# Optimization experiments

Hardware: AMD Instinct MI355X
Metric: run time of the kernel (lower is better)

Reference implementation:

```python
import jax, jax.numpy as jnp
import numpy as np

N_NODES = 10000
N_EDGES = 160000
MUL0 = 16   # multiplicity of 0e irreps
MUL1 = 8    # multiplicity of 1o irreps
H_EDGE = 64
W_NUMEL = MUL0*MUL0 + MUL0*MUL1 + MUL1*MUL1 + MUL1*MUL0  # 576
EPS = 1e-5


def setup_inputs() -> dict:
    key = jax.random.key(0)
    ks = jax.random.split(key, 10)
    atom_features = jax.random.normal(ks[0], (N_NODES, MUL0 + 3*MUL1), dtype=jnp.float32)
    edge_features = jax.random.normal(ks[1], (N_EDGES, H_EDGE), dtype=jnp.float32)
    edge_sh = jax.random.normal(ks[2], (N_EDGES, 4), dtype=jnp.float32)
    edge_index = jax.random.randint(ks[3], (2, N_EDGES), 0, N_NODES, dtype=jnp.int32)
    # fc: Linear(h_edge,h_edge) -> ReLU -> Linear(h_edge, weight_numel)
    fc_w1 = jax.random.normal(ks[4], (H_EDGE, H_EDGE), dtype=jnp.float32) / np.sqrt(H_EDGE).astype(np.float32)
    fc_b1 = jnp.zeros((H_EDGE,), jnp.float32)
    fc_w2 = jax.random.normal(ks[5], (H_EDGE, W_NUMEL), dtype=jnp.float32) / np.sqrt(H_EDGE).astype(np.float32)
    fc_b2 = jnp.zeros((W_NUMEL,), jnp.float32)
    # e3nn BatchNorm affine params: one weight per (mul,irrep) channel, bias only for scalars
    bn_weight = jnp.ones((MUL0 + MUL1,), jnp.float32)
    bn_bias = jnp.zeros((MUL0,), jnp.float32)
    return {"atom_features": atom_features, "edge_features": edge_features,
            "edge_sh": edge_sh, "edge_index": edge_index,
            "fc_w1": fc_w1, "fc_b1": fc_b1, "fc_w2": fc_w2, "fc_b2": fc_b2,
            "bn_weight": bn_weight, "bn_bias": bn_bias}


def _tensor_product(x, edge_sh, w):
    # x: [E, 40] gathered node features; edge_sh: [E, 4]; w: [E, 576] per-edge weights
    E = x.shape[0]
    x0 = x[:, :MUL0]                       # [E,16] scalars 0e
    x1 = x[:, MUL0:].reshape(E, MUL1, 3)   # [E,8,3] vectors 1o
    sh0 = edge_sh[:, 0]                    # [E]
    sh1 = edge_sh[:, 1:4]                  # [E,3]
    i0 = 0
    w11 = w[:, i0:i0+MUL0*MUL0].reshape(E, MUL0, MUL0); i0 += MUL0*MUL0  # 0e x 0e -> 0e
    w12 = w[:, i0:i0+MUL0*MUL1].reshape(E, MUL0, MUL1); i0 += MUL0*MUL1  # 0e x 1o -> 1o
    w13 = w[:, i0:i0+MUL1*MUL1].reshape(E, MUL1, MUL1); i0 += MUL1*MUL1  # 1o x 0e -> 1o
    w14 = w[:, i0:i0+MUL1*MUL0].reshape(E, MUL1, MUL0)                   # 1o x 1o -> 0e (dot)
    inv = lambda f: np.float32(1.0/np.sqrt(f))
    out0 = (jnp.einsum('ei,eij->ej', x0 * sh0[:, None], w11) * inv(MUL0)
            + jnp.einsum('eim,em,eij->ej', x1, sh1, w14) * inv(3*MUL1))
    out1 = (jnp.einsum('ei,em,eij->ejm', x0, sh1, w12) * inv(MUL0)
            + jnp.einsum('eim,eij->ejm', x1 * sh0[:, None, None], w13) * inv(MUL1))
    return jnp.concatenate([out0, out1.reshape(E, MUL1*3)], axis=-1)  # [E,40]


def _batch_norm_irreps(x, bn_weight, bn_bias):
    # e3nn BatchNorm (training mode, batch stats): center+normalize scalars, norm-normalize vectors
    n = x.shape[0]
    s = x[:, :MUL0]                          # [N,16]
    v = x[:, MUL0:].reshape(n, MUL1, 3)      # [N,8,3]
    s = s - s.mean(axis=0)
    s_norm = (s * s).mean(axis=0)            # per scalar channel
    s = s * (jax.lax.rsqrt(s_norm + EPS) * bn_weight[:MUL0]) + bn_bias
    v_norm = (v * v).mean(axis=-1).mean(axis=0)   # per vector channel
    v = v * (jax.lax.rsqrt(v_norm + EPS) * bn_weight[MUL0:])[None, :, None]
    return jnp.concatenate([s, v.reshape(n, MUL1*3)], axis=-1)


def reference(atom_features, edge_features, edge_sh, edge_index,
              fc_w1, fc_b1, fc_w2, fc_b2, bn_weight, bn_bias):
    edge_dst = edge_index[0]
    edge_src = edge_index[1]
    # per-edge TP weights from edge features
    h = jax.nn.relu(edge_features @ fc_w1 + fc_b1)
    w = h @ fc_w2 + fc_b2                              # [E, 576]
    # gather -> tensor product
    tp = _tensor_product(atom_features[edge_dst], edge_sh, w)  # [E,40]
    # scatter_mean over source nodes with dim_size = n_nodes
    sums = jax.ops.segment_sum(tp, edge_src, num_segments=N_NODES)
    cnts = jax.ops.segment_sum(jnp.ones((tp.shape[0],), tp.dtype), edge_src, num_segments=N_NODES)
    out = sums / jnp.maximum(cnts, 1.0)[:, None]
    # residual (in/out irreps have the same dim -> zero padding)
    out = out + atom_features
    out = _batch_norm_irreps(out, bn_weight, bn_bias)
    return out
```

## Files before the change

### kernel.cpp

```cpp
#include <hip/hip_runtime.h>
#include <hip/hip_bf16.h>

#define N_NODES 10000
#define N_EDGES 160000
#define MUL0 16
#define MUL1 8
#define H_EDGE 64
#define W_NUMEL 576
#define EPS 1e-5f

#define BM 32
#define THREADS 256
#define WP 592
#define XS 52
#define CAP 32

#define INV16 0.25f
#define INV24 0.20412414523193154f
#define INV8  0.3535533905932738f

typedef __attribute__((ext_vector_type(8))) short bf16x8;
typedef __attribute__((ext_vector_type(4))) short bf16x4;
typedef __attribute__((ext_vector_type(4))) float f32x4;

__device__ __forceinline__ unsigned short f2bf(float x) {
    __hip_bfloat16 h = __float2bfloat16(x);
    return __builtin_bit_cast(unsigned short, h);
}
__device__ __forceinline__ float bf2f(unsigned short u) {
    union { unsigned int i; float f; } c; c.i = ((unsigned int)u) << 16; return c.f;
}
__device__ __forceinline__ float dot8(bf16x8 w, f32x4 a, f32x4 b) {
    float s = bf2f((unsigned short)w[0]) * a[0];
    s = fmaf(bf2f((unsigned short)w[1]), a[1], s);
    s = fmaf(bf2f((unsigned short)w[2]), a[2], s);
    s = fmaf(bf2f((unsigned short)w[3]), a[3], s);
    s = fmaf(bf2f((unsigned short)w[4]), b[0], s);
    s = fmaf(bf2f((unsigned short)w[5]), b[1], s);
    s = fmaf(bf2f((unsigned short)w[6]), b[2], s);
    s = fmaf(bf2f((unsigned short)w[7]), b[3], s);
    return s;
}

__device__ __forceinline__ int perm_n(int colp) {
    if (colp < 256)      { int jj = colp >> 4,        ii = colp & 15;        return 16 * ii + jj; }
    else if (colp < 384) { int t = colp - 256; int jj = t >> 4, ii = t & 15; return 256 + 8 * ii + jj; }
    else if (colp < 448) { int t = colp - 384; int jj = t >> 3, ii = t & 7;  return 384 + 8 * ii + jj; }
    else                 { int t = colp - 448; int jj = t >> 3, ii = t & 7;  return 448 + 16 * ii + jj; }
}

__global__ __launch_bounds__(256)
void prep_frags(const float* __restrict__ W1, const float* __restrict__ W2,
                const float* __restrict__ b2, const int* __restrict__ e_src,
                unsigned short* __restrict__ W1F, unsigned short* __restrict__ W2F,
                float* __restrict__ b2p, int* __restrict__ cnt_i,
                int* __restrict__ slots)
{
    const int idx = blockIdx.x * 256 + threadIdx.x;
    if (idx < 4096) {
        const int j = idx & 7, l = (idx >> 3) & 63, ks = (idx >> 9) & 1, mt = idx >> 10;
        const int k = 32 * ks + 16 * (j >> 2) + 4 * (l >> 4) + (j & 3);
        const int col = 16 * mt + (l & 15);
        W1F[idx] = f2bf(W1[k * 64 + col]);
    } else if (idx < 4096 + 36864) {
        const int i2 = idx - 4096;
        const int j = i2 & 7, l = (i2 >> 3) & 63, ks = (i2 >> 9) & 1, nt = i2 >> 10;
        const int k = 32 * ks + 16 * (j >> 2) + 4 * (l >> 4) + (j & 3);
        const int colp = 16 * nt + (l & 15);
        W2F[i2] = f2bf(W2[k * 576 + perm_n(colp)]);
    } else if (idx < 4096 + 36864 + 576) {
        const int np = idx - 40960;
        b2p[np] = b2[perm_n(np)];
    }
    if (idx < N_EDGES) {
        const int src = e_src[idx];
        const int pos = atomicAdd(&cnt_i[src], 1);
        if (pos < CAP) slots[src * CAP + pos] = idx;
    }
}

__global__ __launch_bounds__(THREADS)
void fused_edge_kernel(const float* __restrict__ atom,
                       const float* __restrict__ ef,
                       const float* __restrict__ esh,
                       const int*   __restrict__ e_dst,
                       const unsigned short* __restrict__ W1F,
                       const float* __restrict__ b1,
                       const unsigned short* __restrict__ W2F,
                       const float* __restrict__ b2p,
                       unsigned short* __restrict__ tp)
{
    __shared__ __align__(16) unsigned short W_lds[16 * WP];
    __shared__ __align__(16) float xstage[32 * XS];
    __shared__ __align__(16) unsigned short pack_lds[16 * 40];
    unsigned short* ef_lds = W_lds;

    const int tid = threadIdx.x;
    const int l   = tid & 63;
    const int wv  = tid >> 6;
    const int e0  = blockIdx.x * BM;
    const int h4  = l >> 4;
    const int e16 = l & 15;
    const int el  = tid >> 4;
    const int j   = tid & 15;
    const int j8  = j & 7;

    float4 efv[2];
    #pragma unroll
    for (int rr = 0; rr < 2; ++rr) {
        const int i = tid + rr * 256;
        efv[rr] = *(const float4*)(ef + (size_t)(e0 + (i >> 4)) * 64 + (i & 15) * 4);
    }

    int dstP[2]; float4 shvP[2];
    #pragma unroll
    for (int mt = 0; mt < 2; ++mt) {
        const int e = e0 + 16 * mt + el;
        dstP[mt] = e_dst[e];
        shvP[mt] = *(const float4*)(esh + (size_t)e * 4);
    }

    float xjP[2], v0P[2], v1P[2], v2P[2];
    #pragma unroll
    for (int mt = 0; mt < 2; ++mt) {
        const float* x = atom + (size_t)dstP[mt] * 40;
        xjP[mt] = x[j];
        v0P[mt] = x[16 + 3 * j8];
        v1P[mt] = x[17 + 3 * j8];
        v2P[mt] = x[18 + 3 * j8];
    }

    #pragma unroll
    for (int rr = 0; rr < 2; ++rr) {
        const int i    = tid + rr * 256;
        const int edge = i >> 4;
        const int f    = (i & 15) * 4;
        bf16x4 p;
        p[0] = (short)f2bf(efv[rr].x); p[1] = (short)f2bf(efv[rr].y);
        p[2] = (short)f2bf(efv[rr].z); p[3] = (short)f2bf(efv[rr].w);
        const int addr = ((edge << 7) + (f << 1)) ^ ((edge & 7) << 4);
        *(bf16x4*)((char*)ef_lds + addr) = p;
    }
    __syncthreads();

    bf16x8 bH[2][2];
    #pragma unroll
    for (int et = 0; et < 2; ++et) {
        const int edge = 16 * et + e16;
        bf16x8 bE[2];
        #pragma unroll
        for (int ks = 0; ks < 2; ++ks) {
            const int f0 = 32 * ks + 4 * h4;
            const int a0 = ((edge << 7) + (f0 << 1)) ^ ((edge & 7) << 4);
            const int a1 = ((edge << 7) + ((f0 + 16) << 1)) ^ ((edge & 7) << 4);
            bf16x4 lo = *(const bf16x4*)((const char*)ef_lds + a0);
            bf16x4 hi = *(const bf16x4*)((const char*)ef_lds + a1);
            bf16x8 b;
            b[0]=lo[0]; b[1]=lo[1]; b[2]=lo[2]; b[3]=lo[3];
            b[4]=hi[0]; b[5]=hi[1]; b[6]=hi[2]; b[7]=hi[3];
            bE[ks] = b;
        }
        f32x4 accG[4];
        #pragma unroll
        for (int mti = 0; mti < 4; ++mti) {
            accG[mti] = *(const f32x4*)(b1 + 16 * mti + 4 * h4);
            #pragma unroll
            for (int ks = 0; ks < 2; ++ks) {
                const bf16x8 aW = *(const bf16x8*)(W1F + ((size_t)(mti * 2 + ks) * 64 + l) * 8);
                accG[mti] = __builtin_amdgcn_mfma_f32_16x16x32_bf16(aW, bE[ks], accG[mti], 0, 0, 0);
            }
        }
        #pragma unroll
        for (int ks = 0; ks < 2; ++ks) {
            bf16x8 b;
            #pragma unroll
            for (int jj = 0; jj < 4; ++jj) {
                b[jj]     = (short)f2bf(fmaxf(accG[2 * ks    ][jj], 0.0f));
                b[jj + 4] = (short)f2bf(fmaxf(accG[2 * ks + 1][jj], 0.0f));
            }
            bH[et][ks] = b;
        }
    }

    float sh0P[2], s1xP[2], s1yP[2], s1zP[2];
    #pragma unroll
    for (int mt = 0; mt < 2; ++mt) {
        sh0P[mt] = shvP[mt].x; s1xP[mt] = shvP[mt].y;
        s1yP[mt] = shvP[mt].z; s1zP[mt] = shvP[mt].w;
        float* xrow = xstage + (16 * mt + el) * XS;
        xrow[j] = xjP[mt];
        if (j < 8) {
            xrow[16 + j] = v0P[mt] * shvP[mt].y + v1P[mt] * shvP[mt].z + v2P[mt] * shvP[mt].w;
            xrow[24 + j] = v0P[mt];
            xrow[32 + j] = v1P[mt];
            xrow[40 + j] = v2P[mt];
        }
    }
    __syncthreads();

    bf16x4 accb[9][2];
    #pragma unroll
    for (int t = 0; t < 9; ++t) {
        const int nt = 9 * wv + t;
        const f32x4 bias = *(const f32x4*)(b2p + 16 * nt + 4 * h4);
        f32x4 a0 = bias, a1 = bias;
        #pragma unroll
        for (int ks = 0; ks < 2; ++ks) {
            const bf16x8 aW = *(const bf16x8*)(W2F + ((size_t)(nt * 2 + ks) * 64 + l) * 8);
            a0 = __builtin_amdgcn_mfma_f32_16x16x32_bf16(aW, bH[0][ks], a0, 0, 0, 0);
            a1 = __builtin_amdgcn_mfma_f32_16x16x32_bf16(aW, bH[1][ks], a1, 0, 0, 0);
        }
        #pragma unroll
        for (int r = 0; r < 4; ++r) {
            accb[t][0][r] = (short)f2bf(a0[r]);
            accb[t][1][r] = (short)f2bf(a1[r]);
        }
    }

    #pragma unroll
    for (int mt = 0; mt < 2; ++mt) {
        #pragma unroll
        for (int t = 0; t < 9; ++t) {
            const int nt = 9 * wv + t;
            *(bf16x4*)&W_lds[e16 * WP + 16 * nt + 4 * h4] = accb[t][mt];
        }
        __syncthreads();

        const unsigned short* Wt = W_lds + el * WP;
        const float* xv = xstage + (16 * mt + el) * XS;
        const float sh0 = sh0P[mt], s1x = s1xP[mt], s1y = s1yP[mt], s1z = s1zP[mt];

        const bf16x8 t0a = *(const bf16x8*)(Wt + 16 * j);
        const bf16x8 t0b = *(const bf16x8*)(Wt + 16 * j + 8);
        const bf16x8 t3  = *(const bf16x8*)(Wt + 448 + 8 * j);
        const f32x4 xa = *(const f32x4*)(xv);
        const f32x4 xb = *(const f32x4*)(xv + 4);
        const f32x4 xc = *(const f32x4*)(xv + 8);
        const f32x4 xd = *(const f32x4*)(xv + 12);
        const f32x4 d0 = *(const f32x4*)(xv + 16);
        const f32x4 d1 = *(const f32x4*)(xv + 20);
        const float s1 = dot8(t0a, xa, xb) + dot8(t0b, xc, xd);
        const float s2 = dot8(t3, d0, d1);
        pack_lds[el * 40 + j] = f2bf(INV16 * sh0 * s1 + INV24 * s2);
        if (j < 8) {
            const bf16x8 t1a = *(const bf16x8*)(Wt + 256 + 16 * j);
            const bf16x8 t1b = *(const bf16x8*)(Wt + 256 + 16 * j + 8);
            const bf16x8 t2  = *(const bf16x8*)(Wt + 384 + 8 * j);
            const f32x4 v0a = *(const f32x4*)(xv + 24), v0b = *(const f32x4*)(xv + 28);
            const f32x4 v1a = *(const f32x4*)(xv + 32), v1b = *(const f32x4*)(xv + 36);
            const f32x4 v2a = *(const f32x4*)(xv + 40), v2b = *(const f32x4*)(xv + 44);
            const float p  = dot8(t1a, xa, xb) + dot8(t1b, xc, xd);
            const float q0 = dot8(t2, v0a, v0b);
            const float q1 = dot8(t2, v1a, v1b);
            const float q2 = dot8(t2, v2a, v2b);
            const float ps = INV16 * p, qs = INV8 * sh0;
            pack_lds[el * 40 + 16 + 3 * j + 0] = f2bf(s1x * ps + qs * q0);
            pack_lds[el * 40 + 16 + 3 * j + 1] = f2bf(s1y * ps + qs * q1);
            pack_lds[el * 40 + 16 + 3 * j + 2] = f2bf(s1z * ps + qs * q2);
        }
        __syncthreads();

        if (tid < 80) {
            const bf16x8 c = *(const bf16x8*)(pack_lds + 8 * tid);
            *(bf16x8*)(tp + (size_t)(e0 + 16 * mt) * 40 + 8 * tid) = c;
        }
    }
}

__global__ __launch_bounds__(256)
void gather_stats_kernel(const int* __restrict__ cnt_i, const int* __restrict__ slots,
                         const unsigned short* __restrict__ tp, const float* __restrict__ atom,
                         float* __restrict__ y, float* __restrict__ stats)
{
    __shared__ float sred[40];
    const int t0 = blockIdx.x * 256 + threadIdx.x;
    if (threadIdx.x < 40) sred[threadIdx.x] = 0.0f;
    __syncthreads();

    if (t0 < N_NODES * 10) {
        const int n = t0 / 10, g = t0 % 10;
        const int cnt = cnt_i[n];
        const int m = min(cnt, CAP);
        float a0 = 0.f, a1 = 0.f, a2 = 0.f, a3 = 0.f;
        int i = 0;
        for (; i + 4 <= m; i += 4) {
            const int4 e4 = *(const int4*)(slots + n * CAP + i);
            const ushort4 va = *(const ushort4*)(tp + (size_t)e4.x * 40 + 4 * g);
            const ushort4 vb = *(const ushort4*)(tp + (size_t)e4.y * 40 + 4 * g);
            const ushort4 vc = *(const ushort4*)(tp + (size_t)e4.z * 40 + 4 * g);
            const ushort4 vd = *(const ushort4*)(tp + (size_t)e4.w * 40 + 4 * g);
            a0 += bf2f(va.x) + bf2f(vb.x) + bf2f(vc.x) + bf2f(vd.x);
            a1 += bf2f(va.y) + bf2f(vb.y) + bf2f(vc.y) + bf2f(vd.y);
            a2 += bf2f(va.z) + bf2f(vb.z) + bf2f(vc.z) + bf2f(vd.z);
            a3 += bf2f(va.w) + bf2f(vb.w) + bf2f(vc.w) + bf2f(vd.w);
        }
        for (; i < m; ++i) {
            const int eid = slots[n * CAP + i];
            const ushort4 v = *(const ushort4*)(tp + (size_t)eid * 40 + 4 * g);
            a0 += bf2f(v.x); a1 += bf2f(v.y); a2 += bf2f(v.z); a3 += bf2f(v.w);
        }
        const float rinv = 1.0f / (float)max(cnt, 1);
        const float4 av = *(const float4*)(atom + (size_t)n * 40 + 4 * g);
        float o[4];
        o[0] = a0 * rinv + av.x;
        o[1] = a1 * rinv + av.y;
        o[2] = a2 * rinv + av.z;
        o[3] = a3 * rinv + av.w;
        *(float4*)(y + (size_t)n * 40 + 4 * g) = make_float4(o[0], o[1], o[2], o[3]);
        #pragma unroll
        for (int k = 0; k < 4; ++k) {
            const int c = 4 * g + k;
            if (c < 16) {
                atomicAdd(&sred[c], o[k]);
                atomicAdd(&sred[16 + c], o[k] * o[k]);
            } else {
                atomicAdd(&sred[32 + (c - 16) / 3], o[k] * o[k] * (1.0f / 3.0f));
            }
        }
    }
    __syncthreads();
    if (threadIdx.x < 40) atomicAdd(&stats[threadIdx.x], sred[threadIdx.x]);
}

__global__ __launch_bounds__(256)
void apply_bn_kernel(float* __restrict__ y,
                     const float* __restrict__ stats,
                     const float* __restrict__ bnw,
                     const float* __restrict__ bnb)
{
    const int idx = blockIdx.x * blockDim.x + threadIdx.x;
    if (idx >= N_NODES * 10) return;
    const int o0 = (idx * 4) % 40;
    const float invN = 1.0f / (float)N_NODES;
    float4 v = *(float4*)(y + (size_t)idx * 4);
    float* vp = (float*)&v;
    #pragma unroll
    for (int k = 0; k < 4; ++k) {
        const int o = o0 + k;
        if (o < MUL0) {
            const float mean  = stats[o] * invN;
            const float var   = stats[16 + o] * invN - mean * mean;
            const float scale = rsqrtf(var + EPS) * bnw[o];
            vp[k] = (vp[k] - mean) * scale + bnb[o];
        } else {
            const int jj = (o - 16) / 3;
            const float vn = stats[32 + jj] * invN;
            vp[k] = vp[k] * (rsqrtf(vn + EPS) * bnw[16 + jj]);
        }
    }
    *(float4*)(y + (size_t)idx * 4) = v;
}

extern "C" void kernel_launch(void* const* d_in, const int* in_sizes, int n_in,
                              void* d_out, int out_size, void* d_ws, size_t ws_size,
                              hipStream_t stream)
{
    const float* atom = (const float*)d_in[0];
    const float* ef   = (const float*)d_in[1];
    const float* esh  = (const float*)d_in[2];
    const int*   eidx = (const int*)d_in[3];
    const float* W1   = (const float*)d_in[4];
    const float* b1   = (const float*)d_in[5];
    const float* W2   = (const float*)d_in[6];
    const float* b2   = (const float*)d_in[7];
    const float* bnw  = (const float*)d_in[8];
    const float* bnb  = (const float*)d_in[9];
    float* out = (float*)d_out;

    float* stats = (float*)d_ws;
    int*   cnt_i = (int*)d_ws + 40;
    int*   slots = cnt_i + N_NODES;
    float* b2p   = (float*)d_ws + 330048;
    unsigned short* W1F = (unsigned short*)((float*)d_ws + 330624);
    unsigned short* W2F = W1F + 4096;
    unsigned short* tp  = W2F + 36864;

    const int* e_dst = eidx;
    const int* e_src = eidx + N_EDGES;

    hipMemsetAsync(d_ws, 0, (size_t)(40 + N_NODES) * 4, stream);

    prep_frags<<<640, 256, 0, stream>>>(W1, W2, b2, e_src, W1F, W2F, b2p, cnt_i, slots);

    fused_edge_kernel<<<N_EDGES / BM, THREADS, 0, stream>>>(
        atom, ef, esh, e_dst, W1F, b1, W2F, b2p, tp);

    gather_stats_kernel<<<(N_NODES * 10 + 255) / 256, 256, 0, stream>>>(
        cnt_i, slots, tp, atom, out, stats);

    apply_bn_kernel<<<(N_NODES * 10 + 255) / 256, 256, 0, stream>>>(
        out, stats, bnw, bnb);
}
```

Before: 90.65 us.

## Fuse gather-stats and batchnorm apply via cooperative grid sync; reorder w11 columns

Merges the scatter-mean/stats kernel and the batch-norm apply kernel into a single cooperative kernel. A grid-wide sync separates them, so the pre-norm values stay in registers instead of being written out and read back. It also changes the column permutation for the w11 block so each lane reads two contiguous 8-element chunks from LDS. The cost is cooperative launch overhead and a grid barrier across 391 blocks, which must all be co-resident.

```diff
diff --git a/kernel.cpp b/kernel.cpp
--- a/kernel.cpp
+++ b/kernel.cpp
@@ -1,5 +1,7 @@
 #include <hip/hip_runtime.h>
 #include <hip/hip_bf16.h>
+#include <hip/hip_cooperative_groups.h>
+namespace cg = cooperative_groups;
 
 #define N_NODES 10000
 #define N_EDGES 160000
@@ -43,7 +45,8 @@
 }
 
 __device__ __forceinline__ int perm_n(int colp) {
-    if (colp < 256)      { int jj = colp >> 4,        ii = colp & 15;        return 16 * ii + jj; }
+    if (colp < 128)      { int jj = colp >> 3, ii = colp & 7;              return 16 * ii + jj; }
+    else if (colp < 256) { int c = colp - 128; int jj = c >> 3, ii = 8 + (c & 7); return 16 * ii + jj; }
     else if (colp < 384) { int t = colp - 256; int jj = t >> 4, ii = t & 15; return 256 + 8 * ii + jj; }
     else if (colp < 448) { int t = colp - 384; int jj = t >> 3, ii = t & 7;  return 384 + 8 * ii + jj; }
     else                 { int t = colp - 448; int jj = t >> 3, ii = t & 7;  return 448 + 16 * ii + jj; }
@@ -230,8 +233,8 @@
         const float* xv = xstage + (16 * mt + el) * XS;
         const float sh0 = sh0P[mt], s1x = s1xP[mt], s1y = s1yP[mt], s1z = s1zP[mt];
 
-        const bf16x8 t0a = *(const bf16x8*)(Wt + 16 * j);
-        const bf16x8 t0b = *(const bf16x8*)(Wt + 16 * j + 8);
+        const bf16x8 t0a = *(const bf16x8*)(Wt + 8 * j);
+        const bf16x8 t0b = *(const bf16x8*)(Wt + 128 + 8 * j);
         const bf16x8 t3  = *(const bf16x8*)(Wt + 448 + 8 * j);
         const f32x4 xa = *(const f32x4*)(xv);
         const f32x4 xb = *(const f32x4*)(xv + 4);
@@ -268,17 +271,22 @@
 }
 
 __global__ __launch_bounds__(256)
-void gather_stats_kernel(const int* __restrict__ cnt_i, const int* __restrict__ slots,
-                         const unsigned short* __restrict__ tp, const float* __restrict__ atom,
-                         float* __restrict__ y, float* __restrict__ stats)
+void gather_bn_kernel(const int* __restrict__ cnt_i, const int* __restrict__ slots,
+                      const unsigned short* __restrict__ tp, const float* __restrict__ atom,
+                      float* __restrict__ y, float* __restrict__ stats,
+                      const float* __restrict__ bnw, const float* __restrict__ bnb)
 {
     __shared__ float sred[40];
     const int t0 = blockIdx.x * 256 + threadIdx.x;
     if (threadIdx.x < 40) sred[threadIdx.x] = 0.0f;
     __syncthreads();
 
-    if (t0 < N_NODES * 10) {
-        const int n = t0 / 10, g = t0 % 10;
+    const bool active = (t0 < N_NODES * 10);
+    const int n = active ? (t0 / 10) : 0;
+    const int g = active ? (t0 % 10) : 0;
+    float o[4] = {0.f, 0.f, 0.f, 0.f};
+
+    if (active) {
         const int cnt = cnt_i[n];
         const int m = min(cnt, CAP);
         float a0 = 0.f, a1 = 0.f, a2 = 0.f, a3 = 0.f;
@@ -301,12 +309,10 @@
         }
         const float rinv = 1.0f / (float)max(cnt, 1);
         const float4 av = *(const float4*)(atom + (size_t)n * 40 + 4 * g);
-        float o[4];
         o[0] = a0 * rinv + av.x;
         o[1] = a1 * rinv + av.y;
         o[2] = a2 * rinv + av.z;
         o[3] = a3 * rinv + av.w;
-        *(float4*)(y + (size_t)n * 40 + 4 * g) = make_float4(o[0], o[1], o[2], o[3]);
         #pragma unroll
         for (int k = 0; k < 4; ++k) {
             const int c = 4 * g + k;
@@ -320,35 +326,29 @@
     }
     __syncthreads();
     if (threadIdx.x < 40) atomicAdd(&stats[threadIdx.x], sred[threadIdx.x]);
-}
-
-__global__ __launch_bounds__(256)
-void apply_bn_kernel(float* __restrict__ y,
-                     const float* __restrict__ stats,
-                     const float* __restrict__ bnw,
-                     const float* __restrict__ bnb)
-{
-    const int idx = blockIdx.x * blockDim.x + threadIdx.x;
-    if (idx >= N_NODES * 10) return;
-    const int o0 = (idx * 4) % 40;
-    const float invN = 1.0f / (float)N_NODES;
-    float4 v = *(float4*)(y + (size_t)idx * 4);
-    float* vp = (float*)&v;
-    #pragma unroll
-    for (int k = 0; k < 4; ++k) {
-        const int o = o0 + k;
-        if (o < MUL0) {
-            const float mean  = stats[o] * invN;
-            const float var   = stats[16 + o] * invN - mean * mean;
-            const float scale = rsqrtf(var + EPS) * bnw[o];
-            vp[k] = (vp[k] - mean) * scale + bnb[o];
-        } else {
-            const int jj = (o - 16) / 3;
-            const float vn = stats[32 + jj] * invN;
-            vp[k] = vp[k] * (rsqrtf(vn + EPS) * bnw[16 + jj]);
-        }
-    }
-    *(float4*)(y + (size_t)idx * 4) = v;
+
+    cg::this_grid().sync();
+
+    if (active) {
+        const float invN = 1.0f / (float)N_NODES;
+        float4 r;
+        float* rp = (float*)&r;
+        #pragma unroll
+        for (int k = 0; k < 4; ++k) {
+            const int c = 4 * g + k;
+            if (c < 16) {
+                const float mean  = stats[c] * invN;
+                const float var   = stats[16 + c] * invN - mean * mean;
+                const float scale = rsqrtf(var + EPS) * bnw[c];
+                rp[k] = (o[k] - mean) * scale + bnb[c];
+            } else {
+                const int jj = (c - 16) / 3;
+                const float vn = stats[32 + jj] * invN;
+                rp[k] = o[k] * (rsqrtf(vn + EPS) * bnw[16 + jj]);
+            }
+        }
+        *(float4*)(y + (size_t)n * 40 + 4 * g) = r;
+    }
 }
 
 extern "C" void kernel_launch(void* const* d_in, const int* in_sizes, int n_in,
@@ -385,9 +385,11 @@
     fused_edge_kernel<<<N_EDGES / BM, THREADS, 0, stream>>>(
         atom, ef, esh, e_dst, W1F, b1, W2F, b2p, tp);
 
-    gather_stats_kernel<<<(N_NODES * 10 + 255) / 256, 256, 0, stream>>>(
-        cnt_i, slots, tp, atom, out, stats);
-
-    apply_bn_kernel<<<(N_NODES * 10 + 255) / 256, 256, 0, stream>>>(
-        out, stats, bnw, bnb);
-}
+    {
+        void* gb_args[] = { (void*)&cnt_i, (void*)&slots, (void*)&tp, (void*)&atom,
+                            (void*)&out, (void*)&stats, (void*)&bnw, (void*)&bnb };
+        hipLaunchCooperativeKernel((const void*)gather_bn_kernel,
+                                   dim3((N_NODES * 10 + 255) / 256), dim3(256),
+                                   gb_args, 0, stream);
+    }
+}
```

Result: slower. 133.7 us (+47.4%).
